# Kernel tuning notes

Measured on AMD Instinct MI355X. Metric: run time of the kernel, lower is better.

Reference implementation:

```python
import math
import jax, jax.numpy as jnp
import numpy as np

B, L, D_MODEL = 2, 2048, 768
H = 12            # num_heads == num_key_value_heads
FEAT = 16         # feature_dim
HEAD_DIM = D_MODEL // H  # 64


def taylor_exp(x):
    """Taylor-exp feature map: phi(x) = [1, x/rrd, (x (x) x)/(sqrt(2)*rd)].
    x: [..., d] -> [..., 1 + d + d^2]"""
    d = x.shape[-1]
    rd = math.sqrt(d)
    rrd = math.sqrt(rd)
    r2 = math.sqrt(2.0)
    x2 = (x[..., :, None] * x[..., None, :]).reshape(*x.shape[:-1], d * d) / r2
    ones = jnp.ones(x.shape[:-1] + (1,), dtype=x.dtype)
    return jnp.concatenate([ones, x / rrd, x2 / rd], axis=-1)


def setup_inputs() -> dict:
    key = jax.random.key(0)
    k1, k2, k3, k4, k5 = jax.random.split(key, 5)
    s = 0.02
    return {
        "hidden_states": jax.random.normal(k1, (B, L, D_MODEL), jnp.float32),
        "Wq": jax.random.normal(k2, (H * FEAT, D_MODEL), jnp.float32) * s,
        "Wk": jax.random.normal(k3, (H * FEAT, D_MODEL), jnp.float32) * s,
        "Wv": jax.random.normal(k4, (D_MODEL, D_MODEL), jnp.float32) * s,
        "Wo": jax.random.normal(k5, (D_MODEL, D_MODEL), jnp.float32) * s,
    }


def reference(hidden_states, Wq, Wk, Wv, Wo):
    b, l, d = hidden_states.shape
    # projections (torch Linear, no bias): y = x @ W.T
    q = jnp.einsum('bld,fd->blf', hidden_states, Wq).reshape(b, l, H, FEAT).transpose(0, 2, 1, 3)
    k = jnp.einsum('bld,fd->blf', hidden_states, Wk).reshape(b, l, H, FEAT).transpose(0, 2, 1, 3)
    v = jnp.einsum('bld,fd->blf', hidden_states, Wv).reshape(b, l, H, HEAD_DIM).transpose(0, 2, 1, 3)

    q = taylor_exp(q)   # [b,h,l,Dexp]
    k = taylor_exp(k)   # k_enc == k (forward clones k), v_enc == v

    # denominator: k_enc.sum over seq + causal cumsum of k
    k_state = jnp.sum(k, axis=2, keepdims=True) + jnp.cumsum(k, axis=2)  # [b,h,l,Dexp]
    z = 1.0 / jnp.sum(q * k_state, axis=-1)                              # [b,h,l]

    # quadratic scores; y1 uses causal (tril) mask, y2 uses full scores with same k,v
    A = jnp.einsum('bhnd,bhmd->bhnm', q, k)                              # [b,h,l,l]
    causal = jnp.tril(jnp.ones((l, l), dtype=A.dtype))
    A_total = A * causal + A                                             # tril(A) + A
    y = jnp.einsum('bhnm,bhme->bhne', A_total, v) * z[..., None]         # [b,h,l,e]

    out = y.transpose(0, 2, 1, 3).reshape(b, l, H * HEAD_DIM)
    return jnp.einsum('blf,df->bld', out, Wo)
```

## Files before the change

### kernel.cpp

```cpp
#include <hip/hip_runtime.h>

typedef unsigned short ushortT;
typedef __bf16 bf16x8 __attribute__((ext_vector_type(8)));
typedef float f32x4 __attribute__((ext_vector_type(4)));

#define BB   2
#define LL   2048
#define DM   768
#define HH   12
#define FT   16
#define HD   64
#define DEXP 273
#define CH   128
#define NC   16
#define NBH  24
#define NBLK 384
#define C2f  0.17677669529663687f
#define KH   768
#define KP   1536
#define SLAB_US   4096
#define SPK_BLK_US 36864
#define SPK_BLK_B  73728

__device__ __forceinline__ void split_bf16(float x, ushortT& hi, ushortT& lo) {
  unsigned b = __float_as_uint(x);
  unsigned r = b + 0x7FFFu + ((b >> 16) & 1u);
  hi = (ushortT)(r >> 16);
  float hf = __uint_as_float((unsigned)hi << 16);
  lo = (ushortT)(__float_as_uint(x - hf) >> 16);
}

__global__ __launch_bounds__(256) void pack_a(const float* __restrict__ X,
                                              ushortT* __restrict__ Xh,
                                              int total4) {
  int g = blockIdx.x * 256 + threadIdx.x;
  if (g >= total4) return;
  int m = g / 192, k4 = (g % 192) * 4;
  float4 v = *(const float4*)(X + (size_t)m * 768 + k4);
  ushortT h[4], l[4];
  split_bf16(v.x, h[0], l[0]);
  split_bf16(v.y, h[1], l[1]);
  split_bf16(v.z, h[2], l[2]);
  split_bf16(v.w, h[3], l[3]);
  ushortT* p = Xh + (size_t)m * KP + k4;
  *(ushort4*)p = *(ushort4*)h;
  *(ushort4*)(p + KH) = *(ushort4*)l;
}

__global__ __launch_bounds__(256) void pack_w(const float* __restrict__ W0,
                                              const float* __restrict__ W1,
                                              const float* __restrict__ W2,
                                              int n1, int n2,
                                              ushortT* __restrict__ Wh,
                                              int total4) {
  int g = blockIdx.x * 256 + threadIdx.x;
  if (g >= total4) return;
  int n = g / 192, k4 = (g % 192) * 4;
  const float* src = (n < n1 ? W0 + (size_t)n * 768
                    : n < n2 ? W1 + (size_t)(n - n1) * 768
                             : W2 + (size_t)(n - n2) * 768);
  float4 v = *(const float4*)(src + k4);
  ushortT h[4], l[4];
  split_bf16(v.x, h[0], l[0]);
  split_bf16(v.y, h[1], l[1]);
  split_bf16(v.z, h[2], l[2]);
  split_bf16(v.w, h[3], l[3]);
  ushortT* p = Wh + (size_t)n * KP + k4;
  *(ushort4*)p = *(ushort4*)h;
  *(ushort4*)(p + KH) = *(ushort4*)l;
}

typedef const __attribute__((address_space(1))) unsigned gq_t;
typedef __attribute__((address_space(3))) unsigned lq_t;
__device__ __forceinline__ void gload_lds16(const ushortT* g, ushortT* l) {
  __builtin_amdgcn_global_load_lds((gq_t*)g, (lq_t*)l, 16, 0, 0);
}

__global__ __launch_bounds__(256) void mfma_gemm(const ushortT* __restrict__ A,
                                                 const ushortT* __restrict__ B,
                                                 float* __restrict__ Y, int ldy,
                                                 int ntiles) {
  __shared__ ushortT sAh[2][128 * 32], sAl[2][128 * 32];
  __shared__ ushortT sBh[2][64 * 32], sBl[2][64 * 32];
  const int blk = blockIdx.x;
  const int xcd = blk & 7, slot = blk >> 3;
  const int mtp = gridDim.x / (8 * ntiles);
  const int mt = xcd * mtp + slot / ntiles;
  const int nt = slot % ntiles;
  const int bm = mt * 128, bn = nt * 64;
  const int tid = threadIdx.x, wave = tid >> 6, lane = tid & 63;
  const int srow = lane >> 2, schk = (lane & 3) * 8;
  const ushortT* gsrc;
  ushortT* lb0;
  ushortT* lb1;
  int iters;
  switch (wave) {
    case 0:  gsrc = A + (size_t)(bm + srow) * KP + schk;      lb0 = sAh[0]; lb1 = sAh[1]; iters = 8; break;
    case 1:  gsrc = A + (size_t)(bm + srow) * KP + KH + schk; lb0 = sAl[0]; lb1 = sAl[1]; iters = 8; break;
    case 2:  gsrc = B + (size_t)(bn + srow) * KP + schk;      lb0 = sBh[0]; lb1 = sBh[1]; iters = 4; break;
    default: gsrc = B + (size_t)(bn + srow) * KP + KH + schk; lb0 = sBl[0]; lb1 = sBl[1]; iters = 4; break;
  }
  const int wm = (wave & 1) * 64, wn = (wave >> 1) * 32;
  const int fr = lane & 15, quad = lane >> 4;
  f32x4 acc[4][2] = {};
  for (int it = 0; it < iters; it++)
    gload_lds16(gsrc + (size_t)it * 16 * KP, lb0 + it * 512);
  __syncthreads();
#pragma unroll 2
  for (int step = 0; step < 24; step++) {
    const int cur = step & 1;
    if (step < 23) {
      ushortT* lbn = cur ? lb0 : lb1;
      const int k1 = (step + 1) * 32;
      for (int it = 0; it < iters; it++)
        gload_lds16(gsrc + k1 + (size_t)it * 16 * KP, lbn + it * 512);
    }
    const ushortT* pAh = sAh[cur];
    const ushortT* pAl = sAl[cur];
    const ushortT* pBh = sBh[cur];
    const ushortT* pBl = sBl[cur];
    bf16x8 ah[4], al[4], bh2[2], bl2[2];
#pragma unroll
    for (int mi = 0; mi < 4; mi++) {
      ah[mi] = *(const bf16x8*)&pAh[(wm + mi * 16 + fr) * 32 + quad * 8];
      al[mi] = *(const bf16x8*)&pAl[(wm + mi * 16 + fr) * 32 + quad * 8];
    }
#pragma unroll
    for (int ni = 0; ni < 2; ni++) {
      bh2[ni] = *(const bf16x8*)&pBh[(wn + ni * 16 + fr) * 32 + quad * 8];
      bl2[ni] = *(const bf16x8*)&pBl[(wn + ni * 16 + fr) * 32 + quad * 8];
    }
#pragma unroll
    for (int mi = 0; mi < 4; mi++)
#pragma unroll
      for (int ni = 0; ni < 2; ni++) {
        acc[mi][ni] = __builtin_amdgcn_mfma_f32_16x16x32_bf16(ah[mi], bh2[ni], acc[mi][ni], 0, 0, 0);
        acc[mi][ni] = __builtin_amdgcn_mfma_f32_16x16x32_bf16(ah[mi], bl2[ni], acc[mi][ni], 0, 0, 0);
        acc[mi][ni] = __builtin_amdgcn_mfma_f32_16x16x32_bf16(al[mi], bh2[ni], acc[mi][ni], 0, 0, 0);
      }
    __syncthreads();
  }
  const int orow = quad * 4;
#pragma unroll
  for (int mi = 0; mi < 4; mi++)
#pragma unroll
    for (int ni = 0; ni < 2; ni++) {
      float* yp = Y + (size_t)(bm + wm + mi * 16 + orow) * ldy + bn + wn + ni * 16 + fr;
#pragma unroll
      for (int r = 0; r < 4; r++) yp[(size_t)r * ldy] = acc[mi][ni][r];
    }
}

__global__ __launch_bounds__(256, 2) void chunk_sum_kernel(
    const float* __restrict__ qkv, ushortT* __restrict__ Spk,
    float* __restrict__ csk) {
  const int blk = blockIdx.x;
  const int bh = blk >> 4, c = blk & 15;
  const int b = bh / HH, h = bh % HH;
  __shared__ float kT[16][128];
  __shared__ ushortT phiA[288][72];
  __shared__ ushortT Vt[64][72];
  const float* base = qkv + (size_t)(b * LL + c * CH) * 1152;
  const int tid = threadIdx.x;
  const int wave = tid >> 6, lane = tid & 63;
  const int fr = lane & 15, quad = lane >> 4;
  for (int idx = tid; idx < 512; idx += 256) {
    int m = idx >> 2, i4 = (idx & 3) * 4;
    float4 k4 = *(const float4*)&base[(size_t)m * 1152 + 192 + h * 16 + i4];
    kT[i4 + 0][m] = k4.x; kT[i4 + 1][m] = k4.y;
    kT[i4 + 2][m] = k4.z; kT[i4 + 3][m] = k4.w;
  }
  const int wm2 = (wave & 1) * 144, wn2 = (wave >> 1) * 32;
  f32x4 acc[9][2] = {};
  __syncthreads();
#pragma unroll 1
  for (int s = 0; s < 4; s++) {
    const int m0 = s * 32;
    if (s) __syncthreads();
    for (int idx = tid; idx < 512; idx += 256) {
      int m = m0 + (idx >> 4), e4 = (idx & 15) * 4;
      float4 v4 = *(const float4*)&base[(size_t)m * 1152 + 384 + h * 64 + e4];
      ushortT hh[4], ll[4];
      split_bf16(v4.x, hh[0], ll[0]); split_bf16(v4.y, hh[1], ll[1]);
      split_bf16(v4.z, hh[2], ll[2]); split_bf16(v4.w, hh[3], ll[3]);
      const int mi2 = m - m0;
#pragma unroll
      for (int j = 0; j < 4; j++) {
        Vt[e4 + j][mi2] = hh[j];
        Vt[e4 + j][32 + mi2] = ll[j];
      }
    }
    for (int rr = tid; rr < 288; rr += 256) {
      const int f = rr;
      const float* pa = (f >= 17) ? kT[(f - 17) >> 4] : (f >= 1 ? kT[f - 1] : kT[0]);
      const float* pb = (f >= 17) ? kT[(f - 17) & 15] : kT[0];
      const float sc = (f == 0) ? 1.0f : (f < 17 ? 0.5f : C2f);
      const bool quadf = (f >= 17);
      const bool valid = (f < DEXP);
      ushortT hrow[32], lrow[32];
#pragma unroll
      for (int g = 0; g < 8; g++) {
        float4 a4 = *(const float4*)&pa[m0 + g * 4];
        float4 b4 = *(const float4*)&pb[m0 + g * 4];
        float v0, v1, v2, v3;
        if (f == 0) {
          v0 = v1 = v2 = v3 = 1.0f;
        } else if (!quadf) {
          v0 = sc * a4.x; v1 = sc * a4.y; v2 = sc * a4.z; v3 = sc * a4.w;
        } else {
          v0 = sc * a4.x * b4.x; v1 = sc * a4.y * b4.y;
          v2 = sc * a4.z * b4.z; v3 = sc * a4.w * b4.w;
        }
        if (!valid) { v0 = v1 = v2 = v3 = 0.0f; }
        split_bf16(v0, hrow[g * 4 + 0], lrow[g * 4 + 0]);
        split_bf16(v1, hrow[g * 4 + 1], lrow[g * 4 + 1]);
        split_bf16(v2, hrow[g * 4 + 2], lrow[g * 4 + 2]);
        split_bf16(v3, hrow[g * 4 + 3], lrow[g * 4 + 3]);
      }
      *(uint4*)&phiA[f][0] = *(uint4*)&hrow[0];
      *(uint4*)&phiA[f][8] = *(uint4*)&hrow[8];
      *(uint4*)&phiA[f][16] = *(uint4*)&hrow[16];
      *(uint4*)&phiA[f][24] = *(uint4*)&hrow[24];
      *(uint4*)&phiA[f][32] = *(uint4*)&lrow[0];
      *(uint4*)&phiA[f][40] = *(uint4*)&lrow[8];
      *(uint4*)&phiA[f][48] = *(uint4*)&lrow[16];
      *(uint4*)&phiA[f][56] = *(uint4*)&lrow[24];
    }
    __syncthreads();
    bf16x8 bhf[2], blf[2];
#pragma unroll
    for (int ni = 0; ni < 2; ni++) {
      bhf[ni] = *(const bf16x8*)&Vt[wn2 + ni * 16 + fr][quad * 8];
      blf[ni] = *(const bf16x8*)&Vt[wn2 + ni * 16 + fr][32 + quad * 8];
    }
#pragma unroll
    for (int mi = 0; mi < 9; mi++) {
      bf16x8 ah = *(const bf16x8*)&phiA[wm2 + mi * 16 + fr][quad * 8];
      bf16x8 al = *(const bf16x8*)&phiA[wm2 + mi * 16 + fr][32 + quad * 8];
#pragma unroll
      for (int ni = 0; ni < 2; ni++) {
        acc[mi][ni] = __builtin_amdgcn_mfma_f32_16x16x32_bf16(ah, bhf[ni], acc[mi][ni], 0, 0, 0);
        acc[mi][ni] = __builtin_amdgcn_mfma_f32_16x16x32_bf16(ah, blf[ni], acc[mi][ni], 0, 0, 0);
        acc[mi][ni] = __builtin_amdgcn_mfma_f32_16x16x32_bf16(al, bhf[ni], acc[mi][ni], 0, 0, 0);
      }
    }
  }
  for (int f = tid; f < DEXP; f += 256) {
    float sum = 0.0f;
    if (f == 0) {
      sum = (float)CH;
    } else if (f < 17) {
      const float* p = kT[f - 1];
      for (int m = 0; m < CH; m += 4) {
        float4 x = *(const float4*)&p[m];
        sum += x.x + x.y + x.z + x.w;
      }
      sum *= 0.5f;
    } else {
      const float* pa2 = kT[(f - 17) >> 4];
      const float* pb2 = kT[(f - 17) & 15];
      for (int m = 0; m < CH; m += 4) {
        float4 x = *(const float4*)&pa2[m];
        float4 y = *(const float4*)&pb2[m];
        sum += x.x * y.x + x.y * y.y + x.z * y.z + x.w * y.w;
      }
      sum *= C2f;
    }
    csk[(size_t)blk * DEXP + f] = sum;
  }
  __syncthreads();
  ushortT* stage = &phiA[0][0];
  ushortT* Sp = Spk + (size_t)blk * SPK_BLK_US;
#pragma unroll 1
  for (int sl = 0; sl < 9; sl++) {
    if (sl) __syncthreads();
#pragma unroll
    for (int mi = 0; mi < 9; mi++) {
      const int fb = wm2 + mi * 16;
      if ((fb >> 5) == sl) {
        const int fi0 = (fb & 31) + quad * 4;
        const int gh = fi0 >> 3;
        const int inner = (fi0 << 1) & 15;
#pragma unroll
        for (int ni = 0; ni < 2; ni++) {
          const int e = wn2 + ni * 16 + fr;
          const int es = (e & 7) << 4;
          ushortT hh2[4], ll2[4];
#pragma unroll
          for (int r = 0; r < 4; r++) split_bf16(acc[mi][ni][r], hh2[r], ll2[r]);
          char* rowp = (char*)stage + e * 128;
          *(ushort4*)(rowp + ((gh << 4) ^ es) + inner) = *(ushort4*)hh2;
          *(ushort4*)(rowp + (((gh + 4) << 4) ^ es) + inner) = *(ushort4*)ll2;
        }
      }
    }
    __syncthreads();
    uint4* gdst = (uint4*)(Sp + (size_t)sl * SLAB_US);
    const uint4* lsrc = (const uint4*)stage;
    gdst[tid] = lsrc[tid];
    gdst[tid + 256] = lsrc[tid + 256];
  }
}

__global__ __launch_bounds__(256) void prefix_kernel(ushortT* __restrict__ Spk,
                                                     float* __restrict__ csk) {
  const int gid = blockIdx.x * 256 + threadIdx.x;
  const int totS = NBH * 4608;
  if (gid < totS) {
    const int bh = gid / 4608;
    const int rem = gid % 4608;
    const int slab = rem >> 9;
    const int e = (rem >> 3) & 63;
    const int wp = rem & 7;
    const int es = (e & 7) << 4;
    const unsigned off_h = e * 128 + ((((wp >> 1)) << 4) ^ es) + ((wp & 1) << 3);
    const unsigned off_l = e * 128 + ((((wp >> 1) + 4) << 4) ^ es) + ((wp & 1) << 3);
    char* base = (char*)Spk + (size_t)bh * NC * SPK_BLK_B + slab * 8192;
    float r0[NC], r1[NC], r2[NC], r3[NC];
    float t0 = 0.f, t1 = 0.f, t2 = 0.f, t3 = 0.f;
#pragma unroll
    for (int cc = 0; cc < NC; cc++) {
      const char* p = base + (size_t)cc * SPK_BLK_B;
      ushort4 hw = *(const ushort4*)(p + off_h);
      ushort4 lw = *(const ushort4*)(p + off_l);
      r0[cc] = __uint_as_float((unsigned)hw.x << 16) + __uint_as_float((unsigned)lw.x << 16);
      r1[cc] = __uint_as_float((unsigned)hw.y << 16) + __uint_as_float((unsigned)lw.y << 16);
      r2[cc] = __uint_as_float((unsigned)hw.z << 16) + __uint_as_float((unsigned)lw.z << 16);
      r3[cc] = __uint_as_float((unsigned)hw.w << 16) + __uint_as_float((unsigned)lw.w << 16);
      t0 += r0[cc]; t1 += r1[cc]; t2 += r2[cc]; t3 += r3[cc];
    }
    float u0 = 0.f, u1 = 0.f, u2 = 0.f, u3 = 0.f;
#pragma unroll
    for (int cc = 0; cc < NC; cc++) {
      ushort4 hw, lw;
      split_bf16(u0 + t0, hw.x, lw.x);
      split_bf16(u1 + t1, hw.y, lw.y);
      split_bf16(u2 + t2, hw.z, lw.z);
      split_bf16(u3 + t3, hw.w, lw.w);
      char* p = base + (size_t)cc * SPK_BLK_B;
      *(ushort4*)(p + off_h) = hw;
      *(ushort4*)(p + off_l) = lw;
      u0 += r0[cc]; u1 += r1[cc]; u2 += r2[cc]; u3 += r3[cc];
    }
  } else {
    const int g2 = gid - totS;
    if (g2 < NBH * DEXP) {
      const int bh = g2 / DEXP;
      const int f = g2 % DEXP;
      float r[NC];
      float tot = 0.0f;
#pragma unroll
      for (int cc = 0; cc < NC; cc++) {
        r[cc] = csk[(size_t)(bh * NC + cc) * DEXP + f];
        tot += r[cc];
      }
      float run = 0.0f;
#pragma unroll
      for (int cc = 0; cc < NC; cc++) {
        csk[(size_t)(bh * NC + cc) * DEXP + f] = run + tot;
        run += r[cc];
      }
    }
  }
}

__global__ __launch_bounds__(512, 4) void fused_out(
    const float* __restrict__ qkv, const ushortT* __restrict__ Spk,
    const float* __restrict__ csk, ushortT* __restrict__ Ahat) {
  const int blk = blockIdx.x;
  const int bh = blk >> 4, c = blk & 15;
  const int b = bh / HH, h = bh % HH;
  __shared__ ushortT phiA[128][72];
  __shared__ ushortT GtD[2][4096];
  __shared__ ushortT qA1[128][24];
  __shared__ ushortT qA2[128][24];
  __shared__ ushortT kB[32][40];
  __shared__ ushortT gkS[9][64];
  __shared__ ushortT zero64[64];
  __shared__ ushortT onesRow[64];
  __shared__ float zl[128];
  const int tid = threadIdx.x;
  const int wv = tid >> 6, lane = tid & 63;
  const int fr = lane & 15, quad = lane >> 4;
  const int prow = tid >> 2, pq = tid & 3;
  const float* base = qkv + (size_t)(b * LL + c * CH) * 1152;
  const float* qrow = base + (size_t)prow * 1152 + h * 16;
  const ushortT* Gp = Spk + (size_t)blk * SPK_BLK_US;
  float qr[16];
#pragma unroll
  for (int i = 0; i < 4; i++) {
    float4 v = *(const float4*)(qrow + i * 4);
    qr[i * 4 + 0] = v.x; qr[i * 4 + 1] = v.y;
    qr[i * 4 + 2] = v.z; qr[i * 4 + 3] = v.w;
  }
  gload_lds16(Gp + wv * 512 + lane * 8, &GtD[0][wv * 512]);
  {
    ushortT qh4[4], ql4[4];
#pragma unroll
    for (int i = 0; i < 4; i++) split_bf16(qr[pq * 4 + i], qh4[i], ql4[i]);
    *(ushort4*)&qA1[prow][pq * 4] = *(ushort4*)qh4;
    *(ushort4*)&qA2[prow][pq * 4] = *(ushort4*)ql4;
  }
  {
    const float* gkp = csk + (size_t)blk * DEXP;
    for (int f = tid; f < 288; f += 512) {
      float v = (f < DEXP) ? gkp[f] : 0.0f;
      ushortT hh, ll;
      split_bf16(v, hh, ll);
      gkS[f >> 5][f & 31] = hh;
      gkS[f >> 5][32 + (f & 31)] = ll;
    }
  }
  if (tid < 64) {
    zero64[tid] = 0;
    onesRow[tid] = (tid < 32) ? (ushortT)0x3F80 : (ushortT)0;
  }
  f32x4 acc[5] = {};
#pragma unroll 1
  for (int s = 0; s < 9; s++) {
    __syncthreads();
    if (s < 8)
      gload_lds16(Gp + (s + 1) * SLAB_US + wv * 512 + lane * 8,
                  &GtD[(s + 1) & 1][wv * 512]);
    const int f0 = s * 32;
    {
      ushortT h8[8], l8[8];
#pragma unroll
      for (int j = 0; j < 8; j++) {
        const int f = f0 + pq * 8 + j;
        float v;
        if (f == 0) v = 1.0f;
        else if (f < 17) v = 0.5f * qr[f - 1];
        else if (f < DEXP) {
          const int ii = f - 17;
          v = C2f * qr[ii >> 4] * qr[ii & 15];
        } else v = 0.0f;
        split_bf16(v, h8[j], l8[j]);
      }
      *(uint4*)&phiA[prow][pq * 8] = *(uint4*)&h8[0];
      *(uint4*)&phiA[prow][32 + pq * 8] = *(uint4*)&l8[0];
    }
    bf16x8 ah = *(const bf16x8*)&phiA[wv * 16 + fr][quad * 8];
    bf16x8 al = *(const bf16x8*)&phiA[wv * 16 + fr][32 + quad * 8];
    const char* gt = (const char*)&GtD[s & 1][0];
    const int sw = (fr & 7) << 4;
#pragma unroll
    for (int ni = 0; ni < 4; ni++) {
      const int rb = (ni * 16 + fr) * 128;
      bf16x8 bh2 = *(const bf16x8*)(gt + rb + ((quad * 16) ^ sw));
      bf16x8 bl2 = *(const bf16x8*)(gt + rb + ((64 + quad * 16) ^ sw));
      acc[ni] = __builtin_amdgcn_mfma_f32_16x16x32_bf16(ah, bh2, acc[ni], 0, 0, 0);
      acc[ni] = __builtin_amdgcn_mfma_f32_16x16x32_bf16(ah, bl2, acc[ni], 0, 0, 0);
      acc[ni] = __builtin_amdgcn_mfma_f32_16x16x32_bf16(al, bh2, acc[ni], 0, 0, 0);
    }
    {
      const ushortT* gp = (fr == 0) ? &gkS[s][0] : &zero64[0];
      bf16x8 gh = *(const bf16x8*)(gp + quad * 8);
      bf16x8 gl = *(const bf16x8*)(gp + 32 + quad * 8);
      acc[4] = __builtin_amdgcn_mfma_f32_16x16x32_bf16(ah, gh, acc[4], 0, 0, 0);
      acc[4] = __builtin_amdgcn_mfma_f32_16x16x32_bf16(ah, gl, acc[4], 0, 0, 0);
      acc[4] = __builtin_amdgcn_mfma_f32_16x16x32_bf16(al, gh, acc[4], 0, 0, 0);
    }
  }
  __syncthreads();
  ushortT* VtF = &GtD[0][0];
#pragma unroll 1
  for (int s = 0; s < 4; s++) {
    const int m0 = s * 32;
    if (tid < 128) {
      int mL = tid >> 2, i4 = (tid & 3) * 4;
      float4 k4 = *(const float4*)&base[(size_t)(m0 + mL) * 1152 + 192 + h * 16 + i4];
      ushortT hh[4], ll[4];
      split_bf16(k4.x, hh[0], ll[0]); split_bf16(k4.y, hh[1], ll[1]);
      split_bf16(k4.z, hh[2], ll[2]); split_bf16(k4.w, hh[3], ll[3]);
      *(ushort4*)&kB[mL][i4] = *(ushort4*)hh;
      *(ushort4*)&kB[mL][16 + i4] = *(ushort4*)ll;
    }
    {
      int mL = tid >> 4, e4 = (tid & 15) * 4;
      float4 v4 = *(const float4*)&base[(size_t)(m0 + mL) * 1152 + 384 + h * 64 + e4];
      ushortT hh[4], ll[4];
      split_bf16(v4.x, hh[0], ll[0]); split_bf16(v4.y, hh[1], ll[1]);
      split_bf16(v4.z, hh[2], ll[2]); split_bf16(v4.w, hh[3], ll[3]);
#pragma unroll
      for (int j = 0; j < 4; j++) {
        VtF[(e4 + j) * 72 + mL] = hh[j];
        VtF[(e4 + j) * 72 + 32 + mL] = ll[j];
      }
    }
    __syncthreads();
    if (s <= (wv >> 1)) {
      bf16x8 a1 = *(const bf16x8*)&qA1[wv * 16 + fr][(quad & 1) * 8];
      bf16x8 a2 = *(const bf16x8*)&qA2[wv * 16 + fr][(quad & 1) * 8];
#pragma unroll
      for (int mtt = 0; mtt < 2; mtt++) {
        bf16x8 bk = *(const bf16x8*)&kB[mtt * 16 + fr][quad * 8];
        f32x4 sf = {};
        sf = __builtin_amdgcn_mfma_f32_16x16x32_bf16(a1, bk, sf, 0, 0, 0);
        sf = __builtin_amdgcn_mfma_f32_16x16x32_bf16(a2, bk, sf, 0, 0, 0);
        const int mg = m0 + mtt * 16 + fr;
#pragma unroll
        for (int r = 0; r < 4; r++) {
          const int rowL = wv * 16 + quad * 4 + r;
          const float sv = sf[r];
          const float p = (mg <= rowL) ? fmaf(sv, fmaf(sv, 0.03125f, 0.25f), 1.0f) : 0.0f;
          ushortT ph, pl;
          split_bf16(p, ph, pl);
          phiA[rowL][mtt * 16 + fr] = ph;
          phiA[rowL][32 + mtt * 16 + fr] = pl;
        }
      }
      bf16x8 ah = *(const bf16x8*)&phiA[wv * 16 + fr][quad * 8];
      bf16x8 al = *(const bf16x8*)&phiA[wv * 16 + fr][32 + quad * 8];
#pragma unroll
      for (int ni = 0; ni < 4; ni++) {
        bf16x8 bh2 = *(const bf16x8*)&VtF[(ni * 16 + fr) * 72 + quad * 8];
        bf16x8 bl2 = *(const bf16x8*)&VtF[(ni * 16 + fr) * 72 + 32 + quad * 8];
        acc[ni] = __builtin_amdgcn_mfma_f32_16x16x32_bf16(ah, bh2, acc[ni], 0, 0, 0);
        acc[ni] = __builtin_amdgcn_mfma_f32_16x16x32_bf16(ah, bl2, acc[ni], 0, 0, 0);
        acc[ni] = __builtin_amdgcn_mfma_f32_16x16x32_bf16(al, bh2, acc[ni], 0, 0, 0);
      }
      {
        const ushortT* op = (fr == 0) ? &onesRow[0] : &zero64[0];
        bf16x8 oh = *(const bf16x8*)(op + quad * 8);
        acc[4] = __builtin_amdgcn_mfma_f32_16x16x32_bf16(ah, oh, acc[4], 0, 0, 0);
        acc[4] = __builtin_amdgcn_mfma_f32_16x16x32_bf16(al, oh, acc[4], 0, 0, 0);
      }
    }
    __syncthreads();
  }
  if (fr == 0) {
#pragma unroll
    for (int r = 0; r < 4; r++) {
      const int rowL = wv * 16 + quad * 4 + r;
      zl[rowL] = 1.0f / acc[4][r];
    }
  }
  const size_t rowbase = (size_t)(b * LL + c * CH);
#pragma unroll
  for (int ni = 0; ni < 4; ni++)
#pragma unroll
    for (int r = 0; r < 4; r++) {
      const int rowL = wv * 16 + quad * 4 + r;
      const float val = acc[ni][r] * zl[rowL];
      ushortT hh, ll;
      split_bf16(val, hh, ll);
      ushortT* ap = Ahat + (rowbase + rowL) * (size_t)KP + h * 64 + ni * 16 + fr;
      ap[0] = hh;
      ap[KH] = ll;
    }
}

extern "C" void kernel_launch(void* const* d_in, const int* in_sizes, int n_in,
                              void* d_out, int out_size, void* d_ws, size_t ws_size,
                              hipStream_t stream) {
  const float* hs = (const float*)d_in[0];
  const float* Wq = (const float*)d_in[1];
  const float* Wk = (const float*)d_in[2];
  const float* Wv = (const float*)d_in[3];
  const float* Wo = (const float*)d_in[4];
  float* out = (float*)d_out;
  char* ws = (char*)d_ws;
  float* qkv = (float*)(ws);
  char*  attR = ws + 18874368;
  ushortT* Spk = (ushortT*)(ws + 31457280);
  float* csk = (float*)(ws + 59768832);
  ushortT* Xhat = (ushortT*)(ws + 31457280);
  ushortT* What = (ushortT*)attR;
  ushortT* Ahat = (ushortT*)attR;
  ushortT* Wohat = (ushortT*)qkv;
  const dim3 thr(256);
  pack_a<<<3072, thr, 0, stream>>>(hs, Xhat, 4096 * 192);
  pack_w<<<864, thr, 0, stream>>>(Wq, Wk, Wv, 192, 384, What, 1152 * 192);
  mfma_gemm<<<576, thr, 0, stream>>>(Xhat, What, qkv, 1152, 18);
  chunk_sum_kernel<<<NBLK, thr, 0, stream>>>(qkv, Spk, csk);
  {
    const int tot = NBH * 4608 + NBH * DEXP;
    prefix_kernel<<<(tot + 255) / 256, thr, 0, stream>>>(Spk, csk);
  }
  fused_out<<<NBLK, dim3(512), 0, stream>>>(qkv, Spk, csk, Ahat);
  pack_w<<<576, thr, 0, stream>>>(Wo, Wo, Wo, 768, 768, Wohat, 768 * 192);
  mfma_gemm<<<384, thr, 0, stream>>>(Ahat, Wohat, out, DM, 12);
}
```

Measured before the change: 234.5 us.

## Enlarge GEMM N-tile to 128 and stage Ahat stores through LDS

The MFMA GEMM tile grows from 128x64 to 128x128, so each wave computes a 64x64 sub-tile and A-fragment reuse doubles. This halves the grid sizes for both the QKV and output projections. Separately, fused_out now writes its split-bf16 output through a shared-memory staging buffer in two halves, then issues coalesced 16-byte global stores instead of scattered 2-byte stores. The cost is fewer blocks on the GPU (288 and 192), which may leave compute units idle, plus more accumulator registers per thread.

```diff
diff --git a/kernel.cpp b/kernel.cpp
--- a/kernel.cpp
+++ b/kernel.cpp
@@ -81,29 +81,28 @@
                                                  float* __restrict__ Y, int ldy,
                                                  int ntiles) {
   __shared__ ushortT sAh[2][128 * 32], sAl[2][128 * 32];
-  __shared__ ushortT sBh[2][64 * 32], sBl[2][64 * 32];
+  __shared__ ushortT sBh[2][128 * 32], sBl[2][128 * 32];
   const int blk = blockIdx.x;
   const int xcd = blk & 7, slot = blk >> 3;
   const int mtp = gridDim.x / (8 * ntiles);
   const int mt = xcd * mtp + slot / ntiles;
   const int nt = slot % ntiles;
-  const int bm = mt * 128, bn = nt * 64;
+  const int bm = mt * 128, bn = nt * 128;
   const int tid = threadIdx.x, wave = tid >> 6, lane = tid & 63;
   const int srow = lane >> 2, schk = (lane & 3) * 8;
   const ushortT* gsrc;
   ushortT* lb0;
   ushortT* lb1;
-  int iters;
   switch (wave) {
-    case 0:  gsrc = A + (size_t)(bm + srow) * KP + schk;      lb0 = sAh[0]; lb1 = sAh[1]; iters = 8; break;
-    case 1:  gsrc = A + (size_t)(bm + srow) * KP + KH + schk; lb0 = sAl[0]; lb1 = sAl[1]; iters = 8; break;
-    case 2:  gsrc = B + (size_t)(bn + srow) * KP + schk;      lb0 = sBh[0]; lb1 = sBh[1]; iters = 4; break;
-    default: gsrc = B + (size_t)(bn + srow) * KP + KH + schk; lb0 = sBl[0]; lb1 = sBl[1]; iters = 4; break;
-  }
-  const int wm = (wave & 1) * 64, wn = (wave >> 1) * 32;
+    case 0:  gsrc = A + (size_t)(bm + srow) * KP + schk;      lb0 = sAh[0]; lb1 = sAh[1]; break;
+    case 1:  gsrc = A + (size_t)(bm + srow) * KP + KH + schk; lb0 = sAl[0]; lb1 = sAl[1]; break;
+    case 2:  gsrc = B + (size_t)(bn + srow) * KP + schk;      lb0 = sBh[0]; lb1 = sBh[1]; break;
+    default: gsrc = B + (size_t)(bn + srow) * KP + KH + schk; lb0 = sBl[0]; lb1 = sBl[1]; break;
+  }
+  const int wm = (wave & 1) * 64, wn = (wave >> 1) * 64;
   const int fr = lane & 15, quad = lane >> 4;
-  f32x4 acc[4][2] = {};
-  for (int it = 0; it < iters; it++)
+  f32x4 acc[4][4] = {};
+  for (int it = 0; it < 8; it++)
     gload_lds16(gsrc + (size_t)it * 16 * KP, lb0 + it * 512);
   __syncthreads();
 #pragma unroll 2
@@ -112,39 +111,37 @@
     if (step < 23) {
       ushortT* lbn = cur ? lb0 : lb1;
       const int k1 = (step + 1) * 32;
-      for (int it = 0; it < iters; it++)
+      for (int it = 0; it < 8; it++)
         gload_lds16(gsrc + k1 + (size_t)it * 16 * KP, lbn + it * 512);
     }
     const ushortT* pAh = sAh[cur];
     const ushortT* pAl = sAl[cur];
     const ushortT* pBh = sBh[cur];
     const ushortT* pBl = sBl[cur];
-    bf16x8 ah[4], al[4], bh2[2], bl2[2];
+    bf16x8 ah[4], al[4];
 #pragma unroll
     for (int mi = 0; mi < 4; mi++) {
       ah[mi] = *(const bf16x8*)&pAh[(wm + mi * 16 + fr) * 32 + quad * 8];
       al[mi] = *(const bf16x8*)&pAl[(wm + mi * 16 + fr) * 32 + quad * 8];
     }
 #pragma unroll
-    for (int ni = 0; ni < 2; ni++) {
-      bh2[ni] = *(const bf16x8*)&pBh[(wn + ni * 16 + fr) * 32 + quad * 8];
-      bl2[ni] = *(const bf16x8*)&pBl[(wn + ni * 16 + fr) * 32 + quad * 8];
-    }
-#pragma unroll
-    for (int mi = 0; mi < 4; mi++)
-#pragma unroll
-      for (int ni = 0; ni < 2; ni++) {
-        acc[mi][ni] = __builtin_amdgcn_mfma_f32_16x16x32_bf16(ah[mi], bh2[ni], acc[mi][ni], 0, 0, 0);
-        acc[mi][ni] = __builtin_amdgcn_mfma_f32_16x16x32_bf16(ah[mi], bl2[ni], acc[mi][ni], 0, 0, 0);
-        acc[mi][ni] = __builtin_amdgcn_mfma_f32_16x16x32_bf16(al[mi], bh2[ni], acc[mi][ni], 0, 0, 0);
-      }
+    for (int ni = 0; ni < 4; ni++) {
+      bf16x8 bh2 = *(const bf16x8*)&pBh[(wn + ni * 16 + fr) * 32 + quad * 8];
+      bf16x8 bl2 = *(const bf16x8*)&pBl[(wn + ni * 16 + fr) * 32 + quad * 8];
+#pragma unroll
+      for (int mi = 0; mi < 4; mi++) {
+        acc[mi][ni] = __builtin_amdgcn_mfma_f32_16x16x32_bf16(ah[mi], bh2, acc[mi][ni], 0, 0, 0);
+        acc[mi][ni] = __builtin_amdgcn_mfma_f32_16x16x32_bf16(ah[mi], bl2, acc[mi][ni], 0, 0, 0);
+        acc[mi][ni] = __builtin_amdgcn_mfma_f32_16x16x32_bf16(al[mi], bh2, acc[mi][ni], 0, 0, 0);
+      }
+    }
     __syncthreads();
   }
   const int orow = quad * 4;
 #pragma unroll
   for (int mi = 0; mi < 4; mi++)
 #pragma unroll
-    for (int ni = 0; ni < 2; ni++) {
+    for (int ni = 0; ni < 4; ni++) {
       float* yp = Y + (size_t)(bm + wm + mi * 16 + orow) * ldy + bn + wn + ni * 16 + fr;
 #pragma unroll
       for (int r = 0; r < 4; r++) yp[(size_t)r * ldy] = acc[mi][ni][r];
@@ -536,19 +533,38 @@
       zl[rowL] = 1.0f / acc[4][r];
     }
   }
+  ushortT* ost = &phiA[0][0];
   const size_t rowbase = (size_t)(b * LL + c * CH);
 #pragma unroll
-  for (int ni = 0; ni < 4; ni++)
-#pragma unroll
-    for (int r = 0; r < 4; r++) {
-      const int rowL = wv * 16 + quad * 4 + r;
-      const float val = acc[ni][r] * zl[rowL];
-      ushortT hh, ll;
-      split_bf16(val, hh, ll);
-      ushortT* ap = Ahat + (rowbase + rowL) * (size_t)KP + h * 64 + ni * 16 + fr;
-      ap[0] = hh;
-      ap[KH] = ll;
-    }
+  for (int p = 0; p < 2; p++) {
+    __syncthreads();
+    if ((wv >> 2) == p) {
+      const int rloc = (wv & 3) * 16 + quad * 4;
+#pragma unroll
+      for (int ni = 0; ni < 4; ni++)
+#pragma unroll
+        for (int r = 0; r < 4; r++) {
+          const int rowL = wv * 16 + quad * 4 + r;
+          const float val = acc[ni][r] * zl[rowL];
+          ushortT hh, ll;
+          split_bf16(val, hh, ll);
+          ost[(rloc + r) * 144 + ni * 16 + fr] = hh;
+          ost[(rloc + r) * 144 + 72 + ni * 16 + fr] = ll;
+        }
+    }
+    __syncthreads();
+#pragma unroll
+    for (int j = 0; j < 2; j++) {
+      const int idx = tid + j * 512;
+      const int row = idx >> 4;
+      const int g = idx & 15;
+      const int half = g >> 3;
+      const int off = (g & 7) * 8;
+      uint4 v = *(const uint4*)&ost[row * 144 + half * 72 + off];
+      ushortT* ap = Ahat + (rowbase + p * 64 + row) * (size_t)KP + half * KH + h * 64 + off;
+      *(uint4*)ap = v;
+    }
+  }
 }
 
 extern "C" void kernel_launch(void* const* d_in, const int* in_sizes, int n_in,
@@ -572,7 +588,7 @@
   const dim3 thr(256);
   pack_a<<<3072, thr, 0, stream>>>(hs, Xhat, 4096 * 192);
   pack_w<<<864, thr, 0, stream>>>(Wq, Wk, Wv, 192, 384, What, 1152 * 192);
-  mfma_gemm<<<576, thr, 0, stream>>>(Xhat, What, qkv, 1152, 18);
+  mfma_gemm<<<288, thr, 0, stream>>>(Xhat, What, qkv, 1152, 9);
   chunk_sum_kernel<<<NBLK, thr, 0, stream>>>(qkv, Spk, csk);
   {
     const int tot = NBH * 4608 + NBH * DEXP;
@@ -580,5 +596,5 @@
   }
   fused_out<<<NBLK, dim3(512), 0, stream>>>(qkv, Spk, csk, Ahat);
   pack_w<<<576, thr, 0, stream>>>(Wo, Wo, Wo, 768, 768, Wohat, 768 * 192);
-  mfma_gemm<<<384, thr, 0, stream>>>(Ahat, Wohat, out, DM, 12);
-}
+  mfma_gemm<<<192, thr, 0, stream>>>(Ahat, Wohat, out, DM, 6);
+}
```

Measured after the change: 238.1 us. About the same (+1.5%).
